# Performance work log

Measured on AMD Instinct MI355X. Metric: run time of the kernel, lower is better.

Reference implementation:

```python
import jax, jax.numpy as jnp
import numpy as np

SEQ, BATCH, IN_CH = 4096, 8, 256
HID = 256
LOOKBACK, LOOKAHEAD = 1, 0
K = LOOKBACK + 1 + LOOKAHEAD  # conv kernel size = 2


def setup_inputs() -> dict:
    key = jax.random.key(0)
    k1, k2, k3, k4, k5, k6 = jax.random.split(key, 6)
    X = jax.random.normal(k1, (SEQ, BATCH, IN_CH), dtype=jnp.float32)
    hidden = jax.random.normal(k2, (BATCH, HID), dtype=jnp.float32)
    scale = 1.0 / np.sqrt(IN_CH * K)
    Wz = jax.random.normal(k3, (HID, IN_CH, K), dtype=jnp.float32) * scale
    bz = jax.random.normal(k4, (HID,), dtype=jnp.float32) * scale
    Wf = jax.random.normal(k5, (HID, IN_CH, K), dtype=jnp.float32) * scale
    bf = jax.random.normal(k6, (HID,), dtype=jnp.float32) * scale
    return {"X": X, "hidden": hidden, "Wz": Wz, "bz": bz, "Wf": Wf, "bf": bf}


def _conv1d(Xp, W, b):
    # Xp: (B, C_in, S_pad); W: (C_out, C_in, K) -> (B, C_out, S)
    y = jax.lax.conv_general_dilated(
        Xp, W, window_strides=(1,), padding='VALID',
        dimension_numbers=('NCW', 'OIW', 'NCW'))
    return y + b[None, :, None]


def reference(X, hidden, Wz, bz, Wf, bf):
    # pad seq dim: lookback zeros in front, lookahead behind
    X_pad = jnp.pad(X, ((LOOKBACK, LOOKAHEAD), (0, 0), (0, 0)))
    Xp = jnp.transpose(X_pad, (1, 2, 0))  # (B, C_in, S_pad)

    Z = jnp.transpose(_conv1d(Xp, Wz, bz), (2, 0, 1))  # (S, B, H)
    F = jnp.transpose(_conv1d(Xp, Wf, bf), (2, 0, 1))  # (S, B, H)

    Z = Z * jax.nn.sigmoid(1.702 * Z)  # QuickGELU
    F = jax.nn.sigmoid(F)

    def step(h, fz):
        f, z = fz
        h = f * z + (1.0 - f) * h
        return h, h

    h_last, H = jax.lax.scan(step, hidden, (F, Z))
    return H, h_last[None]  # (S,B,H), (1,B,H)
```

## Files before the change

kernel.cpp:

```cpp
#include <hip/hip_runtime.h>


#define SEQn 4096
#define NCH 2048
#define CHUNK 32
#define NCHUNK 128

typedef __attribute__((ext_vector_type(8))) short bf16x8;
typedef __attribute__((ext_vector_type(4))) float floatx4;

__device__ __forceinline__ unsigned short f2bf(float x) {
  unsigned int u = __float_as_uint(x);
  u += 0x7fffu + ((u >> 16) & 1u);
  return (unsigned short)(u >> 16);
}
__device__ __forceinline__ float bf2f(ushort u) {
  return __uint_as_float((unsigned int)u << 16);
}
__device__ __forceinline__ float sigf(float x) {
  return __builtin_amdgcn_rcpf(1.0f + __expf(-x));
}

__global__ void pack_kernel(const float* __restrict__ X,
                            const float* __restrict__ Wz, const float* __restrict__ Wf,
                            ushort* __restrict__ Xbf, ushort* __restrict__ Bm) {
  if (blockIdx.x < 1024) {
    int idx = blockIdx.x * 256 + threadIdx.x;
    int n = idx >> 9, kin = idx & 511;
    const float* W = (n < 256) ? Wz : Wf;
    int h = n & 255, c = kin & 255, tap = kin >> 8;
    Bm[idx] = f2bf(W[h * 512 + c * 2 + tap]);
  } else {
    int idx = (blockIdx.x - 1024) * 256 + threadIdx.x;
    const int total4 = ((SEQn + 1) * NCH) / 4;
    if (idx >= total4) return;
    const int pad4 = NCH / 4;
    float4 v;
    if (idx < pad4) { v.x = 0.f; v.y = 0.f; v.z = 0.f; v.w = 0.f; }
    else v = ((const float4*)X)[idx - pad4];
    ushort4 o;
    o.x = f2bf(v.x); o.y = f2bf(v.y); o.z = f2bf(v.z); o.w = f2bf(v.w);
    ((ushort4*)Xbf)[idx] = o;
  }
}

__global__ __launch_bounds__(256) void gemm_kernel(
    const ushort* __restrict__ Xbf, const ushort* __restrict__ Bm,
    const float* __restrict__ bz, const float* __restrict__ bfb,
    ushort* __restrict__ zout, ushort* __restrict__ fout) {
  __shared__ __align__(16) char smem_raw[32768];
  ushort* sA = (ushort*)smem_raw;
  ushort* sB = (ushort*)(smem_raw + 16384);
  ushort* sT = (ushort*)smem_raw;

  const int tid  = threadIdx.x;
  const int wave = tid >> 6;
  const int lane = tid & 63;
  const int quad = lane >> 4;
  const int lrow = lane & 15;
  const int wm = wave >> 1;
  const int wn = wave & 1;
  const int bm = blockIdx.x;
  const int bn = blockIdx.y;

  floatx4 acc[4][4];
#pragma unroll
  for (int i = 0; i < 4; ++i)
#pragma unroll
    for (int j = 0; j < 4; ++j)
      acc[i][j] = (floatx4){0.f, 0.f, 0.f, 0.f};

  int rowS[4], gko[4];
#pragma unroll
  for (int it = 0; it < 4; ++it) {
    int g = wave * 256 + it * 64 + lane;
    int row = g >> 3, ks8 = g & 7;
    rowS[it] = row;
    gko[it] = (ks8 ^ (row & 7)) * 8;
  }
  char* ldsA = (char*)sA + wave * 4096 + (lane << 4);
  char* ldsB = (char*)sB + wave * 4096 + (lane << 4);

  for (int k0 = 0; k0 < 512; k0 += 64) {
    __syncthreads();
#pragma unroll
    for (int it = 0; it < 4; ++it) {
      const int kk = k0 + gko[it];
      const int cA = (kk < 256) ? kk : kk + 1792;
      __builtin_amdgcn_global_load_lds(
          (const __attribute__((address_space(1))) void*)(Xbf + (size_t)(bm * 128 + rowS[it]) * 256 + cA),
          (__attribute__((address_space(3))) void*)(ldsA + it * 1024), 16, 0, 0);
      __builtin_amdgcn_global_load_lds(
          (const __attribute__((address_space(1))) void*)(Bm + (size_t)(bn * 128 + rowS[it]) * 512 + kk),
          (__attribute__((address_space(3))) void*)(ldsB + it * 1024), 16, 0, 0);
    }
    __syncthreads();

    bf16x8 af[4][2], bfr[4][2];
#pragma unroll
    for (int fi = 0; fi < 4; ++fi) {
      const int r = wm * 64 + fi * 16 + lrow;
#pragma unroll
      for (int ks = 0; ks < 2; ++ks) {
        const int s = (ks * 4 + quad) ^ (r & 7);
        af[fi][ks] = *(const bf16x8*)&sA[r * 64 + s * 8];
      }
    }
#pragma unroll
    for (int fj = 0; fj < 4; ++fj) {
      const int r = wn * 64 + fj * 16 + lrow;
#pragma unroll
      for (int ks = 0; ks < 2; ++ks) {
        const int s = (ks * 4 + quad) ^ (r & 7);
        bfr[fj][ks] = *(const bf16x8*)&sB[r * 64 + s * 8];
      }
    }
#pragma unroll
    for (int ks = 0; ks < 2; ++ks)
#pragma unroll
      for (int fi = 0; fi < 4; ++fi)
#pragma unroll
        for (int fj = 0; fj < 4; ++fj)
          acc[fi][fj] = __builtin_amdgcn_mfma_f32_16x16x32_bf16(af[fi][ks], bfr[fj][ks], acc[fi][fj], 0, 0, 0);
  }

  const bool isZ = (bn < 2);
  ushort* gout = isZ ? zout : fout;
  const int ncol0 = (bn & 1) * 128;
  const float* bias = isZ ? bz : bfb;
  float bv[4];
#pragma unroll
  for (int fj = 0; fj < 4; ++fj)
    bv[fj] = bias[ncol0 + wn * 64 + fj * 16 + lrow];

  for (int round = 0; round < 2; ++round) {
    __syncthreads();
    if (wm == round) {
#pragma unroll
      for (int fi = 0; fi < 4; ++fi)
#pragma unroll
        for (int fj = 0; fj < 4; ++fj)
#pragma unroll
          for (int r = 0; r < 4; ++r) {
            float v = acc[fi][fj][r] + bv[fj];
            float o = isZ ? (v * sigf(1.702f * v)) : sigf(v);
            sT[(fi * 16 + quad * 4 + r) * 136 + wn * 64 + fj * 16 + lrow] = f2bf(o);
          }
    }
    __syncthreads();
#pragma unroll
    for (int it = 0; it < 4; ++it) {
      int e = tid + it * 256;
      int row = e >> 4, seg = e & 15;
      uint4 v = *(uint4*)&sT[row * 136 + seg * 8];
      *(uint4*)(gout + (size_t)(bm * 128 + round * 64 + row) * 256 + ncol0 + seg * 8) = v;
    }
  }
}

__global__ void scanA_kernel(const ushort* __restrict__ z, const ushort* __restrict__ f,
                             float* __restrict__ Ac, float* __restrict__ Cc) {
  int t = blockIdx.x * blockDim.x + threadIdx.x;
  int ch2 = t & 1023;
  int j = t >> 10;
  const size_t base = (size_t)j * CHUNK * NCH + 2 * ch2;
  const ushort* zp = z + base;
  const ushort* fp = f + base;
  float A0 = 1.0f, C0 = 0.0f, A1 = 1.0f, C1 = 0.0f;
#pragma unroll
  for (int i = 0; i < CHUNK; ++i) {
    ushort2 fv = *(const ushort2*)(fp + (size_t)i * NCH);
    ushort2 zv = *(const ushort2*)(zp + (size_t)i * NCH);
    float f0 = bf2f(fv.x), f1 = bf2f(fv.y);
    float a0 = 1.0f - f0, a1 = 1.0f - f1;
    C0 = fmaf(a0, C0, f0 * bf2f(zv.x)); A0 *= a0;
    C1 = fmaf(a1, C1, f1 * bf2f(zv.y)); A1 *= a1;
  }
  float2 Av = {A0, A1}, Cv = {C0, C1};
  *(float2*)(Ac + (size_t)j * NCH + 2 * ch2) = Av;
  *(float2*)(Cc + (size_t)j * NCH + 2 * ch2) = Cv;
}

__global__ void scanB_kernel(const float* __restrict__ hidden,
                             const float* __restrict__ Ac, const float* __restrict__ Cc,
                             float* __restrict__ Hs) {
  const int lane = threadIdx.x & 63;
  const int ch = blockIdx.x * 4 + (threadIdx.x >> 6);
  const int j0 = 2 * lane, j1 = 2 * lane + 1;
  float a0 = Ac[j0 * NCH + ch], c0 = Cc[j0 * NCH + ch];
  float a1 = Ac[j1 * NCH + ch], c1 = Cc[j1 * NCH + ch];
  float a = a0 * a1;
  float c = fmaf(a1, c0, c1);
#pragma unroll
  for (int d = 1; d < 64; d <<= 1) {
    float pa = __shfl_up(a, d, 64);
    float pc = __shfl_up(c, d, 64);
    if (lane >= d) { c = fmaf(a, pc, c); a *= pa; }
  }
  float xa = __shfl_up(a, 1, 64), xc = __shfl_up(c, 1, 64);
  if (lane == 0) { xa = 1.0f; xc = 0.0f; }
  float h0 = hidden[ch];
  float hs0 = fmaf(xa, h0, xc);
  Hs[j0 * NCH + ch] = hs0;
  Hs[j1 * NCH + ch] = fmaf(a0, hs0, c0);
}

__global__ void scanC_kernel(const ushort* __restrict__ z, const ushort* __restrict__ f,
                             const float* __restrict__ Hs, float* __restrict__ out) {
  int t = blockIdx.x * blockDim.x + threadIdx.x;
  int ch2 = t & 1023;
  int j = t >> 10;
  float2 hv = *(const float2*)(Hs + (size_t)j * NCH + 2 * ch2);
  float h0 = hv.x, h1 = hv.y;
  const size_t base = (size_t)j * CHUNK * NCH + 2 * ch2;
  const ushort* zp = z + base;
  const ushort* fp = f + base;
  float* op = out + base;
#pragma unroll
  for (int i = 0; i < CHUNK; ++i) {
    ushort2 fv = *(const ushort2*)(fp + (size_t)i * NCH);
    ushort2 zv = *(const ushort2*)(zp + (size_t)i * NCH);
    float f0 = bf2f(fv.x), f1 = bf2f(fv.y);
    h0 = fmaf(f0, bf2f(zv.x) - h0, h0);
    h1 = fmaf(f1, bf2f(zv.y) - h1, h1);
    float2 o = {h0, h1};
    *(float2*)(op + (size_t)i * NCH) = o;
  }
  if (j == NCHUNK - 1) {
    float2 o = {h0, h1};
    *(float2*)(out + (size_t)SEQn * NCH + 2 * ch2) = o;
  }
}

extern "C" void kernel_launch(void* const* d_in, const int* in_sizes, int n_in,
                              void* d_out, int out_size, void* d_ws, size_t ws_size,
                              hipStream_t stream) {
  const float* X      = (const float*)d_in[0];
  const float* hidden = (const float*)d_in[1];
  const float* Wz     = (const float*)d_in[2];
  const float* bz     = (const float*)d_in[3];
  const float* Wf     = (const float*)d_in[4];
  const float* bfb    = (const float*)d_in[5];
  float* out = (float*)d_out;

  char* ws = (char*)d_ws;
  ushort* zbf = (ushort*)ws;
  ushort* fbf = (ushort*)(ws + 16777216);
  ushort* Xbf = (ushort*)(ws + 33554432);
  ushort* Bm  = (ushort*)(ws + 50335744);
  float* Ac = (float*)(ws + 33554432);
  float* Cc = (float*)(ws + 34603008);
  float* Hs = (float*)(ws + 35651584);

  pack_kernel<<<9218, 256, 0, stream>>>(X, Wz, Wf, Xbf, Bm);
  dim3 ggrid(256, 4);
  gemm_kernel<<<ggrid, 256, 0, stream>>>(Xbf, Bm, bz, bfb, zbf, fbf);
  scanA_kernel<<<512, 256, 0, stream>>>(zbf, fbf, Ac, Cc);
  scanB_kernel<<<512, 256, 0, stream>>>(hidden, Ac, Cc, Hs);
  scanC_kernel<<<512, 256, 0, stream>>>(zbf, fbf, Hs, out);
}
```

Baseline: 145.1 us.

## Fuse three scan kernels with grid barriers and widen GEMM N tile

The three chunked-scan kernels become one persistent kernel of 256 blocks. Agent-scope atomic counters act as grid barriers between the stages, and each thread keeps its z/f chunk in registers so the second pass does not re-read global memory. The GEMM tile grows from 128x128 to 128x256, so one block computes the whole Z or F output width and the B tile doubles in LDS. This removes two launches and one read of z/f. The risks are spin-wait cost, relying on all 256 blocks being co-resident, and more register pressure in both kernels.

```diff
diff --git a/kernel.cpp b/kernel.cpp
--- a/kernel.cpp
+++ b/kernel.cpp
@@ -14,8 +14,11 @@
   u += 0x7fffu + ((u >> 16) & 1u);
   return (unsigned short)(u >> 16);
 }
-__device__ __forceinline__ float bf2f(ushort u) {
-  return __uint_as_float((unsigned int)u << 16);
+__device__ __forceinline__ float bf2f_lo(unsigned int v) {
+  return __uint_as_float(v << 16);
+}
+__device__ __forceinline__ float bf2f_hi(unsigned int v) {
+  return __uint_as_float(v & 0xffff0000u);
 }
 __device__ __forceinline__ float sigf(float x) {
   return __builtin_amdgcn_rcpf(1.0f + __expf(-x));
@@ -23,7 +26,9 @@
 
 __global__ void pack_kernel(const float* __restrict__ X,
                             const float* __restrict__ Wz, const float* __restrict__ Wf,
-                            ushort* __restrict__ Xbf, ushort* __restrict__ Bm) {
+                            ushort* __restrict__ Xbf, ushort* __restrict__ Bm,
+                            unsigned* __restrict__ bar) {
+  if (blockIdx.x == 0 && threadIdx.x == 0) { bar[0] = 0; bar[1] = 0; }
   if (blockIdx.x < 1024) {
     int idx = blockIdx.x * 256 + threadIdx.x;
     int n = idx >> 9, kin = idx & 511;
@@ -44,11 +49,11 @@
   }
 }
 
-__global__ __launch_bounds__(256) void gemm_kernel(
+__global__ __launch_bounds__(256, 2) void gemm_kernel(
     const ushort* __restrict__ Xbf, const ushort* __restrict__ Bm,
     const float* __restrict__ bz, const float* __restrict__ bfb,
     ushort* __restrict__ zout, ushort* __restrict__ fout) {
-  __shared__ __align__(16) char smem_raw[32768];
+  __shared__ __align__(16) char smem_raw[49152];
   ushort* sA = (ushort*)smem_raw;
   ushort* sB = (ushort*)(smem_raw + 16384);
   ushort* sT = (ushort*)smem_raw;
@@ -63,75 +68,79 @@
   const int bm = blockIdx.x;
   const int bn = blockIdx.y;
 
-  floatx4 acc[4][4];
+  floatx4 acc[4][8];
 #pragma unroll
   for (int i = 0; i < 4; ++i)
 #pragma unroll
-    for (int j = 0; j < 4; ++j)
+    for (int j = 0; j < 8; ++j)
       acc[i][j] = (floatx4){0.f, 0.f, 0.f, 0.f};
 
-  int rowS[4], gko[4];
+  int offA[4], koA[4];
 #pragma unroll
   for (int it = 0; it < 4; ++it) {
     int g = wave * 256 + it * 64 + lane;
-    int row = g >> 3, ks8 = g & 7;
-    rowS[it] = row;
-    gko[it] = (ks8 ^ (row & 7)) * 8;
-  }
-  char* ldsA = (char*)sA + wave * 4096 + (lane << 4);
-  char* ldsB = (char*)sB + wave * 4096 + (lane << 4);
+    int row = g >> 3;
+    koA[it] = ((g & 7) ^ (row & 7)) * 8;
+    offA[it] = (bm * 128 + row) * 256;
+  }
+  int offB[8];
+#pragma unroll
+  for (int it = 0; it < 8; ++it) {
+    int g = wave * 512 + it * 64 + lane;
+    int row = g >> 3;
+    offB[it] = (bn * 256 + row) * 512 + ((g & 7) ^ (row & 7)) * 8;
+  }
+  char* ldsA = smem_raw + wave * 4096 + (lane << 4);
+  char* ldsB = smem_raw + 16384 + wave * 8192 + (lane << 4);
 
   for (int k0 = 0; k0 < 512; k0 += 64) {
     __syncthreads();
 #pragma unroll
     for (int it = 0; it < 4; ++it) {
-      const int kk = k0 + gko[it];
+      const int kk = k0 + koA[it];
       const int cA = (kk < 256) ? kk : kk + 1792;
       __builtin_amdgcn_global_load_lds(
-          (const __attribute__((address_space(1))) void*)(Xbf + (size_t)(bm * 128 + rowS[it]) * 256 + cA),
+          (const __attribute__((address_space(1))) void*)(Xbf + offA[it] + cA),
           (__attribute__((address_space(3))) void*)(ldsA + it * 1024), 16, 0, 0);
+    }
+#pragma unroll
+    for (int it = 0; it < 8; ++it) {
       __builtin_amdgcn_global_load_lds(
-          (const __attribute__((address_space(1))) void*)(Bm + (size_t)(bn * 128 + rowS[it]) * 512 + kk),
+          (const __attribute__((address_space(1))) void*)(Bm + offB[it] + k0),
           (__attribute__((address_space(3))) void*)(ldsB + it * 1024), 16, 0, 0);
     }
     __syncthreads();
 
-    bf16x8 af[4][2], bfr[4][2];
-#pragma unroll
-    for (int fi = 0; fi < 4; ++fi) {
-      const int r = wm * 64 + fi * 16 + lrow;
-#pragma unroll
-      for (int ks = 0; ks < 2; ++ks) {
+#pragma unroll
+    for (int ks = 0; ks < 2; ++ks) {
+      bf16x8 af[4], bfr[8];
+#pragma unroll
+      for (int fi = 0; fi < 4; ++fi) {
+        const int r = wm * 64 + fi * 16 + lrow;
         const int s = (ks * 4 + quad) ^ (r & 7);
-        af[fi][ks] = *(const bf16x8*)&sA[r * 64 + s * 8];
+        af[fi] = *(const bf16x8*)&sA[r * 64 + s * 8];
       }
-    }
-#pragma unroll
-    for (int fj = 0; fj < 4; ++fj) {
-      const int r = wn * 64 + fj * 16 + lrow;
-#pragma unroll
-      for (int ks = 0; ks < 2; ++ks) {
+#pragma unroll
+      for (int fj = 0; fj < 8; ++fj) {
+        const int r = wn * 128 + fj * 16 + lrow;
         const int s = (ks * 4 + quad) ^ (r & 7);
-        bfr[fj][ks] = *(const bf16x8*)&sB[r * 64 + s * 8];
+        bfr[fj] = *(const bf16x8*)&sB[r * 64 + s * 8];
       }
-    }
-#pragma unroll
-    for (int ks = 0; ks < 2; ++ks)
 #pragma unroll
       for (int fi = 0; fi < 4; ++fi)
 #pragma unroll
-        for (int fj = 0; fj < 4; ++fj)
-          acc[fi][fj] = __builtin_amdgcn_mfma_f32_16x16x32_bf16(af[fi][ks], bfr[fj][ks], acc[fi][fj], 0, 0, 0);
-  }
-
-  const bool isZ = (bn < 2);
+        for (int fj = 0; fj < 8; ++fj)
+          acc[fi][fj] = __builtin_amdgcn_mfma_f32_16x16x32_bf16(af[fi], bfr[fj], acc[fi][fj], 0, 0, 0);
+    }
+  }
+
+  const bool isZ = (bn == 0);
   ushort* gout = isZ ? zout : fout;
-  const int ncol0 = (bn & 1) * 128;
   const float* bias = isZ ? bz : bfb;
-  float bv[4];
-#pragma unroll
-  for (int fj = 0; fj < 4; ++fj)
-    bv[fj] = bias[ncol0 + wn * 64 + fj * 16 + lrow];
+  float bv[8];
+#pragma unroll
+  for (int fj = 0; fj < 8; ++fj)
+    bv[fj] = bias[wn * 128 + fj * 16 + lrow];
 
   for (int round = 0; round < 2; ++round) {
     __syncthreads();
@@ -139,96 +148,109 @@
 #pragma unroll
       for (int fi = 0; fi < 4; ++fi)
 #pragma unroll
-        for (int fj = 0; fj < 4; ++fj)
-#pragma unroll
-          for (int r = 0; r < 4; ++r) {
-            float v = acc[fi][fj][r] + bv[fj];
-            float o = isZ ? (v * sigf(1.702f * v)) : sigf(v);
-            sT[(fi * 16 + quad * 4 + r) * 136 + wn * 64 + fj * 16 + lrow] = f2bf(o);
-          }
-    }
-    __syncthreads();
-#pragma unroll
-    for (int it = 0; it < 4; ++it) {
+        for (int fj = 0; fj < 8; ++fj)
+#pragma unroll
+        for (int r = 0; r < 4; ++r) {
+          float v = acc[fi][fj][r] + bv[fj];
+          float o = isZ ? (v * sigf(1.702f * v)) : sigf(v);
+          sT[(fi * 16 + quad * 4 + r) * 264 + wn * 128 + fj * 16 + lrow] = f2bf(o);
+        }
+    }
+    __syncthreads();
+#pragma unroll
+    for (int it = 0; it < 8; ++it) {
       int e = tid + it * 256;
-      int row = e >> 4, seg = e & 15;
-      uint4 v = *(uint4*)&sT[row * 136 + seg * 8];
-      *(uint4*)(gout + (size_t)(bm * 128 + round * 64 + row) * 256 + ncol0 + seg * 8) = v;
-    }
-  }
-}
-
-__global__ void scanA_kernel(const ushort* __restrict__ z, const ushort* __restrict__ f,
-                             float* __restrict__ Ac, float* __restrict__ Cc) {
-  int t = blockIdx.x * blockDim.x + threadIdx.x;
-  int ch2 = t & 1023;
-  int j = t >> 10;
+      int row = e >> 5, seg = e & 31;
+      uint4 v = *(uint4*)&sT[row * 264 + seg * 8];
+      *(uint4*)(gout + (size_t)(bm * 128 + round * 64 + row) * 256 + seg * 8) = v;
+    }
+  }
+}
+
+__device__ __forceinline__ void gridbar(unsigned* ctr, unsigned target) {
+  __syncthreads();
+  if (threadIdx.x == 0) {
+    __hip_atomic_fetch_add(ctr, 1u, __ATOMIC_ACQ_REL, __HIP_MEMORY_SCOPE_AGENT);
+    while (__hip_atomic_load(ctr, __ATOMIC_ACQUIRE, __HIP_MEMORY_SCOPE_AGENT) < target)
+      __builtin_amdgcn_s_sleep(8);
+  }
+  __syncthreads();
+}
+
+__global__ __launch_bounds__(512, 2) void scan_kernel(
+    const ushort* __restrict__ z, const ushort* __restrict__ f,
+    const float* __restrict__ hidden,
+    float* __restrict__ Ac, float* __restrict__ Cc, float* __restrict__ Hs,
+    float* __restrict__ out, unsigned* __restrict__ bar) {
+  const int tid = threadIdx.x;
+  const int t = blockIdx.x * 512 + tid;
+  const int ch2 = t & 1023;
+  const int j = t >> 10;
   const size_t base = (size_t)j * CHUNK * NCH + 2 * ch2;
-  const ushort* zp = z + base;
-  const ushort* fp = f + base;
+
+  unsigned zr[CHUNK], fr[CHUNK];
   float A0 = 1.0f, C0 = 0.0f, A1 = 1.0f, C1 = 0.0f;
 #pragma unroll
   for (int i = 0; i < CHUNK; ++i) {
-    ushort2 fv = *(const ushort2*)(fp + (size_t)i * NCH);
-    ushort2 zv = *(const ushort2*)(zp + (size_t)i * NCH);
-    float f0 = bf2f(fv.x), f1 = bf2f(fv.y);
+    unsigned fv = *(const unsigned*)(f + base + (size_t)i * NCH);
+    unsigned zv = *(const unsigned*)(z + base + (size_t)i * NCH);
+    fr[i] = fv; zr[i] = zv;
+    float f0 = bf2f_lo(fv), f1 = bf2f_hi(fv);
     float a0 = 1.0f - f0, a1 = 1.0f - f1;
-    C0 = fmaf(a0, C0, f0 * bf2f(zv.x)); A0 *= a0;
-    C1 = fmaf(a1, C1, f1 * bf2f(zv.y)); A1 *= a1;
-  }
-  float2 Av = {A0, A1}, Cv = {C0, C1};
-  *(float2*)(Ac + (size_t)j * NCH + 2 * ch2) = Av;
-  *(float2*)(Cc + (size_t)j * NCH + 2 * ch2) = Cv;
-}
-
-__global__ void scanB_kernel(const float* __restrict__ hidden,
-                             const float* __restrict__ Ac, const float* __restrict__ Cc,
-                             float* __restrict__ Hs) {
-  const int lane = threadIdx.x & 63;
-  const int ch = blockIdx.x * 4 + (threadIdx.x >> 6);
-  const int j0 = 2 * lane, j1 = 2 * lane + 1;
-  float a0 = Ac[j0 * NCH + ch], c0 = Cc[j0 * NCH + ch];
-  float a1 = Ac[j1 * NCH + ch], c1 = Cc[j1 * NCH + ch];
-  float a = a0 * a1;
-  float c = fmaf(a1, c0, c1);
-#pragma unroll
-  for (int d = 1; d < 64; d <<= 1) {
-    float pa = __shfl_up(a, d, 64);
-    float pc = __shfl_up(c, d, 64);
-    if (lane >= d) { c = fmaf(a, pc, c); a *= pa; }
-  }
-  float xa = __shfl_up(a, 1, 64), xc = __shfl_up(c, 1, 64);
-  if (lane == 0) { xa = 1.0f; xc = 0.0f; }
-  float h0 = hidden[ch];
-  float hs0 = fmaf(xa, h0, xc);
-  Hs[j0 * NCH + ch] = hs0;
-  Hs[j1 * NCH + ch] = fmaf(a0, hs0, c0);
-}
-
-__global__ void scanC_kernel(const ushort* __restrict__ z, const ushort* __restrict__ f,
-                             const float* __restrict__ Hs, float* __restrict__ out) {
-  int t = blockIdx.x * blockDim.x + threadIdx.x;
-  int ch2 = t & 1023;
-  int j = t >> 10;
-  float2 hv = *(const float2*)(Hs + (size_t)j * NCH + 2 * ch2);
-  float h0 = hv.x, h1 = hv.y;
-  const size_t base = (size_t)j * CHUNK * NCH + 2 * ch2;
-  const ushort* zp = z + base;
-  const ushort* fp = f + base;
-  float* op = out + base;
-#pragma unroll
-  for (int i = 0; i < CHUNK; ++i) {
-    ushort2 fv = *(const ushort2*)(fp + (size_t)i * NCH);
-    ushort2 zv = *(const ushort2*)(zp + (size_t)i * NCH);
-    float f0 = bf2f(fv.x), f1 = bf2f(fv.y);
-    h0 = fmaf(f0, bf2f(zv.x) - h0, h0);
-    h1 = fmaf(f1, bf2f(zv.y) - h1, h1);
-    float2 o = {h0, h1};
-    *(float2*)(op + (size_t)i * NCH) = o;
-  }
-  if (j == NCHUNK - 1) {
-    float2 o = {h0, h1};
-    *(float2*)(out + (size_t)SEQn * NCH + 2 * ch2) = o;
+    C0 = fmaf(a0, C0, f0 * bf2f_lo(zv)); A0 *= a0;
+    C1 = fmaf(a1, C1, f1 * bf2f_hi(zv)); A1 *= a1;
+  }
+  {
+    const size_t o = (size_t)j * NCH + 2 * ch2;
+    __hip_atomic_store(Ac + o,     A0, __ATOMIC_RELEASE, __HIP_MEMORY_SCOPE_AGENT);
+    __hip_atomic_store(Ac + o + 1, A1, __ATOMIC_RELEASE, __HIP_MEMORY_SCOPE_AGENT);
+    __hip_atomic_store(Cc + o,     C0, __ATOMIC_RELEASE, __HIP_MEMORY_SCOPE_AGENT);
+    __hip_atomic_store(Cc + o + 1, C1, __ATOMIC_RELEASE, __HIP_MEMORY_SCOPE_AGENT);
+  }
+  gridbar(bar, 256);
+
+  {
+    const int lane = tid & 63;
+    const int ch = blockIdx.x * 8 + (tid >> 6);
+    const int j0 = 2 * lane, j1 = 2 * lane + 1;
+    float a0 = __hip_atomic_load(Ac + (size_t)j0 * NCH + ch, __ATOMIC_ACQUIRE, __HIP_MEMORY_SCOPE_AGENT);
+    float c0 = __hip_atomic_load(Cc + (size_t)j0 * NCH + ch, __ATOMIC_ACQUIRE, __HIP_MEMORY_SCOPE_AGENT);
+    float a1 = __hip_atomic_load(Ac + (size_t)j1 * NCH + ch, __ATOMIC_ACQUIRE, __HIP_MEMORY_SCOPE_AGENT);
+    float c1 = __hip_atomic_load(Cc + (size_t)j1 * NCH + ch, __ATOMIC_ACQUIRE, __HIP_MEMORY_SCOPE_AGENT);
+    float a = a0 * a1;
+    float c = fmaf(a1, c0, c1);
+#pragma unroll
+    for (int d = 1; d < 64; d <<= 1) {
+      float pa = __shfl_up(a, d, 64);
+      float pc = __shfl_up(c, d, 64);
+      if (lane >= d) { c = fmaf(a, pc, c); a *= pa; }
+    }
+    float xa = __shfl_up(a, 1, 64), xc = __shfl_up(c, 1, 64);
+    if (lane == 0) { xa = 1.0f; xc = 0.0f; }
+    float h0 = hidden[ch];
+    float hs0 = fmaf(xa, h0, xc);
+    __hip_atomic_store(Hs + (size_t)j0 * NCH + ch, hs0, __ATOMIC_RELEASE, __HIP_MEMORY_SCOPE_AGENT);
+    __hip_atomic_store(Hs + (size_t)j1 * NCH + ch, fmaf(a0, hs0, c0), __ATOMIC_RELEASE, __HIP_MEMORY_SCOPE_AGENT);
+  }
+  gridbar(bar + 1, 256);
+
+  {
+    const size_t o = (size_t)j * NCH + 2 * ch2;
+    float h0 = __hip_atomic_load(Hs + o,     __ATOMIC_ACQUIRE, __HIP_MEMORY_SCOPE_AGENT);
+    float h1 = __hip_atomic_load(Hs + o + 1, __ATOMIC_ACQUIRE, __HIP_MEMORY_SCOPE_AGENT);
+    float* op = out + base;
+#pragma unroll
+    for (int i = 0; i < CHUNK; ++i) {
+      unsigned fv = fr[i], zv = zr[i];
+      h0 = fmaf(bf2f_lo(fv), bf2f_lo(zv) - h0, h0);
+      h1 = fmaf(bf2f_hi(fv), bf2f_hi(zv) - h1, h1);
+      float2 ov = {h0, h1};
+      *(float2*)(op + (size_t)i * NCH) = ov;
+    }
+    if (j == NCHUNK - 1) {
+      float2 ov = {h0, h1};
+      *(float2*)(out + (size_t)SEQn * NCH + 2 * ch2) = ov;
+    }
   }
 }
 
@@ -248,14 +270,13 @@
   ushort* fbf = (ushort*)(ws + 16777216);
   ushort* Xbf = (ushort*)(ws + 33554432);
   ushort* Bm  = (ushort*)(ws + 50335744);
+  unsigned* bar = (unsigned*)(ws + 50860032);
   float* Ac = (float*)(ws + 33554432);
   float* Cc = (float*)(ws + 34603008);
   float* Hs = (float*)(ws + 35651584);
 
-  pack_kernel<<<9218, 256, 0, stream>>>(X, Wz, Wf, Xbf, Bm);
-  dim3 ggrid(256, 4);
+  pack_kernel<<<9218, 256, 0, stream>>>(X, Wz, Wf, Xbf, Bm, bar);
+  dim3 ggrid(256, 2);
   gemm_kernel<<<ggrid, 256, 0, stream>>>(Xbf, Bm, bz, bfb, zbf, fbf);
-  scanA_kernel<<<512, 256, 0, stream>>>(zbf, fbf, Ac, Cc);
-  scanB_kernel<<<512, 256, 0, stream>>>(hidden, Ac, Cc, Hs);
-  scanC_kernel<<<512, 256, 0, stream>>>(zbf, fbf, Hs, out);
-}
+  scan_kernel<<<256, 512, 0, stream>>>(zbf, fbf, hidden, Ac, Cc, Hs, out, bar);
+}
```

After: 371.4 us. 156% more time.

## Double-buffer GEMM K-loop and halve scan chunk length for more parallelism

Applied to the files above, without the earlier changes.

The GEMM main loop switches from single-buffered 64-wide K steps with two barriers to double-buffered 32-wide K steps. The next tile is prefetched into the other LDS buffer while MFMAs run on the current one, so each step needs one barrier. Separately, the scan chunk size drops from 32 to 16, doubling the chunk count and the scanA/scanC grids. scanB now combines four chunk partials per lane and the workspace offsets grow to match. The cost is more, shorter K iterations, a longer sequential pass in scanB, and more traffic for the chunk partials.

```diff
diff --git a/kernel.cpp b/kernel.cpp
--- a/kernel.cpp
+++ b/kernel.cpp
@@ -3,8 +3,8 @@
 
 #define SEQn 4096
 #define NCH 2048
-#define CHUNK 32
-#define NCHUNK 128
+#define CHUNK 16
+#define NCHUNK 256
 
 typedef __attribute__((ext_vector_type(8))) short bf16x8;
 typedef __attribute__((ext_vector_type(4))) float floatx4;
@@ -49,8 +49,6 @@
     const float* __restrict__ bz, const float* __restrict__ bfb,
     ushort* __restrict__ zout, ushort* __restrict__ fout) {
   __shared__ __align__(16) char smem_raw[32768];
-  ushort* sA = (ushort*)smem_raw;
-  ushort* sB = (ushort*)(smem_raw + 16384);
   ushort* sT = (ushort*)smem_raw;
 
   const int tid  = threadIdx.x;
@@ -70,58 +68,71 @@
     for (int j = 0; j < 4; ++j)
       acc[i][j] = (floatx4){0.f, 0.f, 0.f, 0.f};
 
-  int rowS[4], gko[4];
-#pragma unroll
-  for (int it = 0; it < 4; ++it) {
-    int g = wave * 256 + it * 64 + lane;
-    int row = g >> 3, ks8 = g & 7;
+  int rowS[2], gko[2];
+#pragma unroll
+  for (int it = 0; it < 2; ++it) {
+    int g = it * 256 + wave * 64 + lane;
+    int row = g >> 2, ks4 = g & 3;
     rowS[it] = row;
-    gko[it] = (ks8 ^ (row & 7)) * 8;
-  }
-  char* ldsA = (char*)sA + wave * 4096 + (lane << 4);
-  char* ldsB = (char*)sB + wave * 4096 + (lane << 4);
-
-  for (int k0 = 0; k0 < 512; k0 += 64) {
-    __syncthreads();
-#pragma unroll
-    for (int it = 0; it < 4; ++it) {
-      const int kk = k0 + gko[it];
-      const int cA = (kk < 256) ? kk : kk + 1792;
-      __builtin_amdgcn_global_load_lds(
-          (const __attribute__((address_space(1))) void*)(Xbf + (size_t)(bm * 128 + rowS[it]) * 256 + cA),
-          (__attribute__((address_space(3))) void*)(ldsA + it * 1024), 16, 0, 0);
-      __builtin_amdgcn_global_load_lds(
-          (const __attribute__((address_space(1))) void*)(Bm + (size_t)(bn * 128 + rowS[it]) * 512 + kk),
-          (__attribute__((address_space(3))) void*)(ldsB + it * 1024), 16, 0, 0);
-    }
-    __syncthreads();
-
-    bf16x8 af[4][2], bfr[4][2];
+    gko[it] = (ks4 ^ (row & 3)) * 8;
+  }
+  char* ldsA = smem_raw + wave * 1024 + (lane << 4);
+  char* ldsB = smem_raw + 8192 + wave * 1024 + (lane << 4);
+
+#pragma unroll
+  for (int it = 0; it < 2; ++it) {
+    const int kk = gko[it];
+    __builtin_amdgcn_global_load_lds(
+        (const __attribute__((address_space(1))) void*)(Xbf + (size_t)(bm * 128 + rowS[it]) * 256 + kk),
+        (__attribute__((address_space(3))) void*)(ldsA + it * 4096), 16, 0, 0);
+    __builtin_amdgcn_global_load_lds(
+        (const __attribute__((address_space(1))) void*)(Bm + (size_t)(bn * 128 + rowS[it]) * 512 + kk),
+        (__attribute__((address_space(3))) void*)(ldsB + it * 4096), 16, 0, 0);
+  }
+  __syncthreads();
+
+#pragma unroll
+  for (int k = 0; k < 16; ++k) {
+    const int cur = k & 1;
+    const int bo = cur * 16384;
+
+    bf16x8 af[4], bfr[4];
 #pragma unroll
     for (int fi = 0; fi < 4; ++fi) {
       const int r = wm * 64 + fi * 16 + lrow;
-#pragma unroll
-      for (int ks = 0; ks < 2; ++ks) {
-        const int s = (ks * 4 + quad) ^ (r & 7);
-        af[fi][ks] = *(const bf16x8*)&sA[r * 64 + s * 8];
-      }
+      const int s = quad ^ (r & 3);
+      af[fi] = *(const bf16x8*)(smem_raw + bo + r * 64 + s * 16);
     }
 #pragma unroll
     for (int fj = 0; fj < 4; ++fj) {
       const int r = wn * 64 + fj * 16 + lrow;
-#pragma unroll
-      for (int ks = 0; ks < 2; ++ks) {
-        const int s = (ks * 4 + quad) ^ (r & 7);
-        bfr[fj][ks] = *(const bf16x8*)&sB[r * 64 + s * 8];
+      const int s = quad ^ (r & 3);
+      bfr[fj] = *(const bf16x8*)(smem_raw + bo + 8192 + r * 64 + s * 16);
+    }
+
+    if (k < 15) {
+      const int nbo = (cur ^ 1) * 16384;
+      const int k0 = (k + 1) * 32;
+#pragma unroll
+      for (int it = 0; it < 2; ++it) {
+        const int kk = k0 + gko[it];
+        const int cA = (kk < 256) ? kk : kk + 1792;
+        __builtin_amdgcn_global_load_lds(
+            (const __attribute__((address_space(1))) void*)(Xbf + (size_t)(bm * 128 + rowS[it]) * 256 + cA),
+            (__attribute__((address_space(3))) void*)(ldsA + nbo + it * 4096), 16, 0, 0);
+        __builtin_amdgcn_global_load_lds(
+            (const __attribute__((address_space(1))) void*)(Bm + (size_t)(bn * 128 + rowS[it]) * 512 + kk),
+            (__attribute__((address_space(3))) void*)(ldsB + nbo + it * 4096), 16, 0, 0);
       }
     }
-#pragma unroll
-    for (int ks = 0; ks < 2; ++ks)
-#pragma unroll
-      for (int fi = 0; fi < 4; ++fi)
-#pragma unroll
-        for (int fj = 0; fj < 4; ++fj)
-          acc[fi][fj] = __builtin_amdgcn_mfma_f32_16x16x32_bf16(af[fi][ks], bfr[fj][ks], acc[fi][fj], 0, 0, 0);
+
+#pragma unroll
+    for (int fi = 0; fi < 4; ++fi)
+#pragma unroll
+      for (int fj = 0; fj < 4; ++fj)
+        acc[fi][fj] = __builtin_amdgcn_mfma_f32_16x16x32_bf16(af[fi], bfr[fj], acc[fi][fj], 0, 0, 0);
+
+    __syncthreads();
   }
 
   const bool isZ = (bn < 2);
@@ -186,11 +197,15 @@
                              float* __restrict__ Hs) {
   const int lane = threadIdx.x & 63;
   const int ch = blockIdx.x * 4 + (threadIdx.x >> 6);
-  const int j0 = 2 * lane, j1 = 2 * lane + 1;
-  float a0 = Ac[j0 * NCH + ch], c0 = Cc[j0 * NCH + ch];
-  float a1 = Ac[j1 * NCH + ch], c1 = Cc[j1 * NCH + ch];
-  float a = a0 * a1;
-  float c = fmaf(a1, c0, c1);
+  float al[4], cl[4];
+#pragma unroll
+  for (int i = 0; i < 4; ++i) {
+    al[i] = Ac[(size_t)(4 * lane + i) * NCH + ch];
+    cl[i] = Cc[(size_t)(4 * lane + i) * NCH + ch];
+  }
+  float a = al[0], c = cl[0];
+#pragma unroll
+  for (int i = 1; i < 4; ++i) { c = fmaf(al[i], c, cl[i]); a *= al[i]; }
 #pragma unroll
   for (int d = 1; d < 64; d <<= 1) {
     float pa = __shfl_up(a, d, 64);
@@ -199,10 +214,12 @@
   }
   float xa = __shfl_up(a, 1, 64), xc = __shfl_up(c, 1, 64);
   if (lane == 0) { xa = 1.0f; xc = 0.0f; }
-  float h0 = hidden[ch];
-  float hs0 = fmaf(xa, h0, xc);
-  Hs[j0 * NCH + ch] = hs0;
-  Hs[j1 * NCH + ch] = fmaf(a0, hs0, c0);
+  float h = fmaf(xa, hidden[ch], xc);
+#pragma unroll
+  for (int i = 0; i < 4; ++i) {
+    Hs[(size_t)(4 * lane + i) * NCH + ch] = h;
+    h = fmaf(al[i], h, cl[i]);
+  }
 }
 
 __global__ void scanC_kernel(const ushort* __restrict__ z, const ushort* __restrict__ f,
@@ -249,13 +266,13 @@
   ushort* Xbf = (ushort*)(ws + 33554432);
   ushort* Bm  = (ushort*)(ws + 50335744);
   float* Ac = (float*)(ws + 33554432);
-  float* Cc = (float*)(ws + 34603008);
-  float* Hs = (float*)(ws + 35651584);
+  float* Cc = (float*)(ws + 35651584);
+  float* Hs = (float*)(ws + 37748736);
 
   pack_kernel<<<9218, 256, 0, stream>>>(X, Wz, Wf, Xbf, Bm);
   dim3 ggrid(256, 4);
   gemm_kernel<<<ggrid, 256, 0, stream>>>(Xbf, Bm, bz, bfb, zbf, fbf);
-  scanA_kernel<<<512, 256, 0, stream>>>(zbf, fbf, Ac, Cc);
+  scanA_kernel<<<1024, 256, 0, stream>>>(zbf, fbf, Ac, Cc);
   scanB_kernel<<<512, 256, 0, stream>>>(hidden, Ac, Cc, Hs);
-  scanC_kernel<<<512, 256, 0, stream>>>(zbf, fbf, Hs, out);
-}
+  scanC_kernel<<<1024, 256, 0, stream>>>(zbf, fbf, Hs, out);
+}
```

Measured after the change: 150.4 us. 1.04x slower.
